# Kernel tuning notes

Hardware: AMD Instinct MI355X
Metric: run time of the kernel (lower is better)

Reference implementation:

```python
import jax, jax.numpy as jnp
import numpy as np

N = 2048       # num nodes
IN = 512       # in_features == hidden_features == out_features (residuals)
HID = 512
OUT = 512
H = 8          # num_heads
DX = 256       # x feature dim
LN_EPS = 1e-5
NORM_EPS = 1e-12


def _layernorm(x, g, b):
    mu = jnp.mean(x, axis=-1, keepdims=True)
    var = jnp.mean(jnp.square(x - mu), axis=-1, keepdims=True)
    return (x - mu) * jax.lax.rsqrt(var + LN_EPS) * g + b


def _l1_normalize(x):
    # torch F.normalize(p=1): x / max(||x||_1, eps)
    n = jnp.sum(jnp.abs(x), axis=-1, keepdims=True)
    return x / jnp.maximum(n, NORM_EPS)


def _linear_init(key, out_f, in_f):
    kw, kb = jax.random.split(key)
    bound = 1.0 / np.sqrt(in_f)
    W = jax.random.uniform(kw, (out_f, in_f), jnp.float32, -bound, bound)
    b = jax.random.uniform(kb, (out_f,), jnp.float32, -bound, bound)
    return W, b


def setup_inputs() -> dict:
    key = jax.random.key(0)
    ks = jax.random.split(key, 10)
    h = jax.random.normal(ks[0], (N, IN), jnp.float32)
    x = jax.random.uniform(ks[1], (N, DX), jnp.float32)
    Wk, bk = _linear_init(ks[2], HID, IN)
    Wq, bq = _linear_init(ks[3], HID, IN)
    Wv, bv = _linear_init(ks[4], HID, IN)
    Wm1, bm1 = _linear_init(ks[5], H, H + 1)   # mixing_x2h
    Wm2, bm2 = _linear_init(ks[6], 1, H)
    Wfc, bfc = _linear_init(ks[7], OUT, HID + 4)
    ln_g = jnp.ones((IN,), jnp.float32)
    ln_b = jnp.zeros((IN,), jnp.float32)
    lnf_g = jnp.ones((HID,), jnp.float32)
    lnf_b = jnp.zeros((HID,), jnp.float32)
    return dict(h=h, x=x, ln_g=ln_g, ln_b=ln_b, Wk=Wk, bk=bk, Wq=Wq, bq=bq,
                Wv=Wv, bv=bv, Wm1=Wm1, bm1=bm1, Wm2=Wm2, bm2=bm2,
                lnf_g=lnf_g, lnf_b=lnf_b, Wfc=Wfc, bfc=bfc)


def reference(h, x, ln_g, ln_b, Wk, bk, Wq, bq, Wv, bv, Wm1, bm1, Wm2, bm2,
              lnf_g, lnf_b, Wfc, bfc):
    h0, x0 = h, x
    hn = _layernorm(h, ln_g, ln_b)
    xn = _l1_normalize(x)

    k = (hn @ Wk.T + bk).reshape(N, HID // H, H)
    q = (hn @ Wq.T + bq).reshape(N, HID // H, H)
    a_h = jnp.einsum('xyb,zyb->xzb', k, q)          # [N, N, H]
    a_x = xn @ xn.T                                  # [N, N]

    # head mixing: Linear(H+1 -> H) over concat([a_x, a_h])
    a_cat = jnp.concatenate([a_x[..., None], a_h], axis=-1)  # [N, N, H+1]
    a_h = a_cat @ Wm1.T + bm1                                # [N, N, H]
    a_x = (a_h @ Wm2.T + bm2)[..., 0] + a_x                  # [N, N]

    a_h = jax.nn.softmax(a_h, axis=-1)               # softmax over heads
    a_x = _l1_normalize(a_x)

    # per-row stats of a_x -> [N, 4]
    i = jnp.concatenate([
        jnp.diagonal(a_x)[:, None],
        jnp.sum(a_x, axis=-1, keepdims=True),
        jnp.std(a_x, axis=-1, ddof=1, keepdims=True),
        jnp.max(a_x, axis=-1, keepdims=True),
    ], axis=-1)

    v = (hn @ Wv.T + bv).reshape(N, OUT // H, H)
    hm = jnp.einsum('xyb,yzb->xzb', a_h, v).reshape(N, HID)
    xm = a_x @ xn

    hm = hm + h0
    xm = xm + x0
    _h0 = hm

    hf = _layernorm(hm, lnf_g, lnf_b)
    hf = jnp.concatenate([hf, i], axis=-1)           # [N, HID+4]
    hf = jax.nn.elu(hf @ Wfc.T + bfc)
    hf = hf + _h0
    return (hf, xm)
```

## Files before the change

kernel.cpp:

```cpp
#include <hip/hip_runtime.h>
#include <math.h>

#define NN 2048
#define FD 512
#define DXF 256
#define JC 8
#define CHKJ (NN/JC)
#define ITI 32
#define JTW 64
#define NIT (CHKJ/JTW)
#define KC (NN/4)

typedef unsigned short u16;
typedef unsigned int u32;
typedef __attribute__((ext_vector_type(8))) short s16x8;
typedef __attribute__((ext_vector_type(4))) float f32x4;

__device__ __forceinline__ f32x4 MFMA16(s16x8 a, s16x8 b, f32x4 c) {
  return __builtin_amdgcn_mfma_f32_16x16x32_bf16(a, b, c, 0, 0, 0);
}
__device__ __forceinline__ float blo(u32 u) { return __uint_as_float(u << 16); }
__device__ __forceinline__ float bhi(u32 u) { return __uint_as_float(u & 0xffff0000u); }
__device__ __forceinline__ float b2f(u16 v) { return __uint_as_float((u32)v << 16); }
__device__ __forceinline__ u16 bf1(float f) {
  u32 u = __float_as_uint(f);
  u += 0x7fffu + ((u >> 16) & 1u);
  return (u16)(u >> 16);
}
__device__ __forceinline__ u32 pkbf(float a, float b) {
  u32 ua = __float_as_uint(a), ub = __float_as_uint(b);
  ua += 0x7fffu + ((ua >> 16) & 1u);
  ub += 0x7fffu + ((ub >> 16) & 1u);
  return (ua >> 16) | (ub & 0xffff0000u);
}

__global__ void preproc_k(
    const float* __restrict__ h, const float* __restrict__ ln_g,
    const float* __restrict__ ln_b, u16* __restrict__ hnB,
    const float* __restrict__ x, u16* __restrict__ xnB,
    const float* __restrict__ Wk, const float* __restrict__ Wq,
    const float* __restrict__ Wv, u16* __restrict__ wkB, u16* __restrict__ wqB,
    u16* __restrict__ wvB, const float* __restrict__ Wfc, u16* __restrict__ wfcB) {
  int bid = blockIdx.x, t = threadIdx.x;
  __shared__ float red[4][2];
  if (bid < NN) {
    int r = bid;
    float2 v = ((const float2*)(h + (size_t)r * FD))[t];
    float2 w = make_float2(v.x + v.y, v.x * v.x + v.y * v.y);
#pragma unroll
    for (int o = 32; o > 0; o >>= 1) { w.x += __shfl_xor(w.x, o); w.y += __shfl_xor(w.y, o); }
    if ((t & 63) == 0) { red[t >> 6][0] = w.x; red[t >> 6][1] = w.y; }
    __syncthreads();
    float S  = (red[0][0] + red[1][0]) + (red[2][0] + red[3][0]);
    float SQ = (red[0][1] + red[1][1]) + (red[2][1] + red[3][1]);
    float mean = S * (1.f / FD);
    float var  = SQ * (1.f / FD) - mean * mean;
    float rs = rsqrtf(var + 1e-5f);
    float2 gg = ((const float2*)ln_g)[t], bb = ((const float2*)ln_b)[t];
    float ox = (v.x - mean) * rs * gg.x + bb.x;
    float oy = (v.y - mean) * rs * gg.y + bb.y;
    *(u32*)(hnB + (size_t)r * FD + 2 * t) = pkbf(ox, oy);
  } else if (bid < 2 * NN) {
    int r = bid - NN;
    float v = x[(size_t)r * DXF + t];
    float s = fabsf(v);
#pragma unroll
    for (int o = 32; o > 0; o >>= 1) s += __shfl_xor(s, o);
    if ((t & 63) == 0) red[t >> 6][0] = s;
    __syncthreads();
    float S = (red[0][0] + red[1][0]) + (red[2][0] + red[3][0]);
    float inv = 1.f / fmaxf(S, 1e-12f);
    xnB[(size_t)r * DXF + t] = bf1(v * inv);
  } else if (bid < 2 * NN + 1536) {
    int idx = bid - 2 * NN;
    int z = idx >> 9;
    int i = ((idx & 511) << 8) + t;
    const float* W = (z == 0) ? Wk : (z == 1) ? Wq : Wv;
    u16* O = (z == 0) ? wkB : (z == 1) ? wqB : wvB;
    float2 v = ((const float2*)W)[i];
    ((u32*)O)[i] = pkbf(v.x, v.y);
  } else {
    int i = (bid - (2 * NN + 1536)) * 256 + t;
    if (i < 512 * 272) {
      int r = i / 272, c2 = (i - r * 272) * 2;
      float a = (c2 < 516) ? Wfc[r * 516 + c2] : 0.f;
      float b = (c2 + 1 < 516) ? Wfc[r * 516 + c2 + 1] : 0.f;
      ((u32*)wfcB)[i] = pkbf(a, b);
    }
  }
}

__global__ void xnt_k(const u16* __restrict__ xnB, u16* __restrict__ xnTg) {
  __shared__ u16 tile[16][264];
  int t = threadIdx.x;
  int r0 = blockIdx.x * 16;
#pragma unroll
  for (int s = 0; s < 2; ++s) {
    int c = s * 256 + t;
    int db = c & 31, row = c >> 5;
    *(uint4*)&tile[row][db * 8] = *(const uint4*)(xnB + (size_t)(r0 + row) * DXF + db * 8);
  }
  __syncthreads();
#pragma unroll
  for (int s = 0; s < 2; ++s) {
    int c = s * 256 + t;
    int jb = c & 1, d = c >> 1;
    u32 p[4];
#pragma unroll
    for (int e2 = 0; e2 < 4; ++e2) {
      u16 a = tile[jb * 8 + e2 * 2][d], b = tile[jb * 8 + e2 * 2 + 1][d];
      p[e2] = (u32)a | ((u32)b << 16);
    }
    *(uint4*)(xnTg + (size_t)d * NN + r0 + jb * 8) = make_uint4(p[0], p[1], p[2], p[3]);
  }
}

__global__ __launch_bounds__(256) void proj3_k(
    const u16* __restrict__ A,
    const u16* __restrict__ W0, const u16* __restrict__ W1, const u16* __restrict__ W2,
    const float* __restrict__ b0, const float* __restrict__ b1, const float* __restrict__ b2,
    u16* __restrict__ kP, u16* __restrict__ qP, u16* __restrict__ vPT) {
  int z = blockIdx.z;
  const u16* B = (z == 0) ? W0 : (z == 1) ? W1 : W2;
  const float* bias = (z == 0) ? b0 : (z == 1) ? b1 : b2;
  int t = threadIdx.x, w = t >> 6, lane = t & 63, g = lane >> 4, li = lane & 15;
  int m0 = blockIdx.x * 64 + (w & 1) * 32;
  int n0 = blockIdx.y * 64 + (w >> 1) * 32;
  f32x4 acc[2][2] = {};
  for (int k0 = 0; k0 < FD; k0 += 32) {
    s16x8 a0 = *(const s16x8*)(A + (size_t)(m0 + li) * FD + k0 + g * 8);
    s16x8 a1 = *(const s16x8*)(A + (size_t)(m0 + 16 + li) * FD + k0 + g * 8);
    s16x8 bA = *(const s16x8*)(B + (size_t)(n0 + li) * FD + k0 + g * 8);
    s16x8 bB = *(const s16x8*)(B + (size_t)(n0 + 16 + li) * FD + k0 + g * 8);
    acc[0][0] = MFMA16(a0, bA, acc[0][0]);
    acc[0][1] = MFMA16(a0, bB, acc[0][1]);
    acc[1][0] = MFMA16(a1, bA, acc[1][0]);
    acc[1][1] = MFMA16(a1, bB, acc[1][1]);
  }
#pragma unroll
  for (int ms = 0; ms < 2; ++ms)
#pragma unroll
    for (int ns = 0; ns < 2; ++ns) {
      int ncol = n0 + ns * 16 + li;
      float bv = bias[ncol];
      if (z < 2) {
        u16* out = z ? qP : kP;
#pragma unroll
        for (int r = 0; r < 4; ++r) {
          int i = m0 + ms * 16 + g * 4 + r;
          out[((size_t)(ncol & 7) * NN + i) * 64 + (ncol >> 3)] = bf1(acc[ms][ns][r] + bv);
        }
      } else {
        u16 e[4];
#pragma unroll
        for (int r = 0; r < 4; ++r) e[r] = bf1(acc[ms][ns][r] + bv);
        u32 p0 = (u32)e[0] | ((u32)e[1] << 16);
        u32 p1 = (u32)e[2] | ((u32)e[3] << 16);
        int ib = m0 + ms * 16 + g * 4;
        *(uint2*)(vPT + ((size_t)((ncol & 7) * 64 + (ncol >> 3))) * NN + ib) =
            make_uint2(p0, p1);
      }
    }
}

__global__ __launch_bounds__(256) void fc_gemm_k(
    const u16* __restrict__ A, const u16* __restrict__ B,
    const float* __restrict__ bias, const float* __restrict__ res,
    float* __restrict__ C) {
  int t = threadIdx.x, w = t >> 6, lane = t & 63, g = lane >> 4, li = lane & 15;
  int m0 = blockIdx.x * 32 + (w & 1) * 16;
  int n0 = blockIdx.y * 32 + (w >> 1) * 16;
  f32x4 acc = {};
  for (int k0 = 0; k0 < 544; k0 += 32) {
    s16x8 a0 = *(const s16x8*)(A + (size_t)(m0 + li) * 544 + k0 + g * 8);
    s16x8 b0 = *(const s16x8*)(B + (size_t)(n0 + li) * 544 + k0 + g * 8);
    acc = MFMA16(a0, b0, acc);
  }
  int ncol = n0 + li;
  float bv = bias[ncol];
#pragma unroll
  for (int r = 0; r < 4; ++r) {
    int i = m0 + g * 4 + r;
    float cv = acc[r] + bv;
    cv = (cv > 0.f) ? cv : (expf(cv) - 1.f);
    cv += res[(size_t)i * FD + ncol];
    C[(size_t)i * FD + ncol] = cv;
  }
}

__global__ __launch_bounds__(256) void xm_split_k(
    const u16* __restrict__ axg, const u16* __restrict__ xnTg,
    float* __restrict__ xmp, float* __restrict__ stq) {
  int t = threadIdx.x, w = t >> 6, lane = t & 63, g = lane >> 4, li = lane & 15;
  int m0 = blockIdx.x * 64 + (w & 1) * 32;
  int n0 = blockIdx.y * 64 + (w >> 1) * 32;
  int z = blockIdx.z;
  const int kb = z * KC;
  f32x4 acc[2][2] = {};
  float sab[2] = {0.f, 0.f}, ssu[2] = {0.f, 0.f}, ssq[2] = {0.f, 0.f};
  float smx[2] = {-1e30f, -1e30f};
  const bool do_stats = (blockIdx.y == 0) && ((w >> 1) == 0);
  for (int k0 = 0; k0 < KC; k0 += 32) {
    s16x8 a0 = *(const s16x8*)(axg + (size_t)(m0 + li) * NN + kb + k0 + g * 8);
    s16x8 a1 = *(const s16x8*)(axg + (size_t)(m0 + 16 + li) * NN + kb + k0 + g * 8);
    s16x8 bA = *(const s16x8*)(xnTg + (size_t)(n0 + li) * NN + kb + k0 + g * 8);
    s16x8 bB = *(const s16x8*)(xnTg + (size_t)(n0 + 16 + li) * NN + kb + k0 + g * 8);
    acc[0][0] = MFMA16(a0, bA, acc[0][0]);
    acc[0][1] = MFMA16(a0, bB, acc[0][1]);
    acc[1][0] = MFMA16(a1, bA, acc[1][0]);
    acc[1][1] = MFMA16(a1, bB, acc[1][1]);
    if (do_stats) {
#pragma unroll
      for (int ms = 0; ms < 2; ++ms) {
        u32 pu[4];
        *(s16x8*)pu = ms ? a1 : a0;
#pragma unroll
        for (int q2 = 0; q2 < 4; ++q2) {
          float x0 = blo(pu[q2]), x1 = bhi(pu[q2]);
          sab[ms] += fabsf(x0) + fabsf(x1);
          ssu[ms] += x0 + x1;
          ssq[ms] += x0 * x0 + x1 * x1;
          smx[ms] = fmaxf(smx[ms], fmaxf(x0, x1));
        }
      }
    }
  }
  if (do_stats) {
#pragma unroll
    for (int off = 16; off < 64; off <<= 1) {
#pragma unroll
      for (int ms = 0; ms < 2; ++ms) {
        sab[ms] += __shfl_xor(sab[ms], off);
        ssu[ms] += __shfl_xor(ssu[ms], off);
        ssq[ms] += __shfl_xor(ssq[ms], off);
        smx[ms] = fmaxf(smx[ms], __shfl_xor(smx[ms], off));
      }
    }
    if (g == 0) {
#pragma unroll
      for (int ms = 0; ms < 2; ++ms) {
        size_t base = ((size_t)z * NN + m0 + ms * 16 + li) * 4;
        stq[base + 0] = sab[ms]; stq[base + 1] = ssu[ms];
        stq[base + 2] = ssq[ms]; stq[base + 3] = smx[ms];
      }
    }
  }
#pragma unroll
  for (int ms = 0; ms < 2; ++ms)
#pragma unroll
    for (int ns = 0; ns < 2; ++ns) {
      int ncol = n0 + ns * 16 + li;
#pragma unroll
      for (int r = 0; r < 4; ++r) {
        int i = m0 + ms * 16 + g * 4 + r;
        xmp[(size_t)z * NN * DXF + (size_t)i * DXF + ncol] = acc[ms][ns][r];
      }
    }
}

__global__ __launch_bounds__(512, 4) void fused_mfma_k(
    const u16* __restrict__ kP, const u16* __restrict__ qP,
    const u16* __restrict__ vPT, const u16* __restrict__ xnB,
    const float* __restrict__ Wm1, const float* __restrict__ bm1,
    const float* __restrict__ Wm2, const float* __restrict__ bm2,
    u16* __restrict__ hmPart, u16* __restrict__ axg, float* __restrict__ stPd) {
  __shared__ __align__(16) unsigned char L[81920];
  const int O_KI = 0, O_XNI = 32768, O_P = 49152;
  const int t = threadIdx.x, w = t >> 6, lane = t & 63;
  const int g = lane >> 4, li = lane & 15;
  const int i0 = blockIdx.x * ITI, chunk = blockIdx.y;
  const int si = w & 1;
  const int jL = (w >> 1) * 16 + li;
  const int iRow = si * 16 + li;

  float W1[8][9], B1v[8], w2v[8];
#pragma unroll
  for (int o = 0; o < 8; ++o) {
    B1v[o] = bm1[o];
    w2v[o] = Wm2[o];
#pragma unroll
    for (int b3 = 0; b3 < 9; ++b3) W1[o][b3] = Wm1[o * 9 + b3];
  }
  const float b2v = bm2[0];

#pragma unroll
  for (int s = 0; s < 4; ++s) {
    int c = s * 512 + t;
    int yb = c & 7, il = (c >> 3) & 31, b = c >> 8;
    uint4 v = *(const uint4*)(kP + ((size_t)b * NN + i0 + il) * 64 + yb * 8);
    *(uint4*)(L + O_KI + b * 4096 + il * 128 + ((yb ^ (il & 7)) << 4)) = v;
  }
#pragma unroll
  for (int s = 0; s < 2; ++s) {
    int c = s * 512 + t;
    int db = c & 31, il = c >> 5;
    uint4 v = *(const uint4*)(xnB + (size_t)(i0 + il) * DXF + db * 8);
    *(uint4*)(L + O_XNI + il * 512 + ((db ^ (il & 7)) << 4)) = v;
  }
  __syncthreads();

  f32x4 hmA[2][4];
#pragma unroll
  for (int a = 0; a < 2; ++a)
#pragma unroll
    for (int c = 0; c < 4; ++c) hmA[a][c] = (f32x4)(0.f);

  for (int it = 0; it < NIT; ++it) {
    const int j0 = chunk * CHKJ + it * JTW;
    f32x4 accS[9];
#pragma unroll
    for (int a = 0; a < 9; ++a) accS[a] = (f32x4)(0.f);
#pragma unroll
    for (int b = 0; b < 8; ++b)
#pragma unroll
      for (int ks = 0; ks < 2; ++ks) {
        int blk = ks * 4 + g;
        s16x8 af = *(const s16x8*)(L + O_KI + b * 4096 + iRow * 128 +
                                   ((blk ^ (iRow & 7)) << 4));
        s16x8 bf = *(const s16x8*)(qP + ((size_t)b * NN + j0 + jL) * 64 + ks * 32 + g * 8);
        accS[b] = MFMA16(af, bf, accS[b]);
      }
#pragma unroll
    for (int ks = 0; ks < 8; ++ks) {
      int blk = ks * 4 + g;
      s16x8 af = *(const s16x8*)(L + O_XNI + iRow * 512 + ((blk ^ (iRow & 7)) << 4));
      s16x8 bf = *(const s16x8*)(xnB + (size_t)(j0 + jL) * DXF + ks * 32 + g * 8);
      accS[8] = MFMA16(af, bf, accS[8]);
    }
    __syncthreads();
#pragma unroll
    for (int r = 0; r < 4; ++r) {
      float sb[8];
#pragma unroll
      for (int b = 0; b < 8; ++b) sb[b] = accS[b][r];
      float ax = accS[8][r];
      float m[8];
#pragma unroll
      for (int o = 0; o < 8; ++o) {
        float a = B1v[o] + W1[o][0] * ax;
#pragma unroll
        for (int b = 0; b < 8; ++b) a += W1[o][1 + b] * sb[b];
        m[o] = a;
      }
      float axn = b2v + ax;
#pragma unroll
      for (int o = 0; o < 8; ++o) axn += w2v[o] * m[o];
      const int iL2 = si * 16 + g * 4 + r;
      const int iG = i0 + iL2, jG = j0 + jL;
      axg[(size_t)iG * NN + jG] = bf1(axn);
      if (iG == jG) stPd[iG] = axn;
      float mx = m[0];
#pragma unroll
      for (int o = 1; o < 8; ++o) mx = fmaxf(mx, m[o]);
      float es[8], esum = 0.f;
#pragma unroll
      for (int o = 0; o < 8; ++o) { es[o] = __expf(m[o] - mx); esum += es[o]; }
      float inv = 1.f / esum;
      const int base = iL2 * 128 + (((jL >> 3) ^ (iL2 & 7)) << 4) + (jL & 7) * 2;
#pragma unroll
      for (int b = 0; b < 8; ++b)
        *(u16*)(L + O_P + b * 4096 + base) = bf1(es[b] * inv);
    }
    __syncthreads();
#pragma unroll
    for (int hh = 0; hh < 2; ++hh) {
      const int hd = (w >> 1) * 2 + hh;
#pragma unroll
      for (int kb = 0; kb < 2; ++kb) {
        const int prow = si * 16 + li;
        s16x8 pa = *(const s16x8*)(L + O_P + hd * 4096 + prow * 128 +
                                   (((kb * 4 + g) ^ (prow & 7)) << 4));
#pragma unroll
        for (int zt = 0; zt < 4; ++zt) {
          s16x8 vf = *(const s16x8*)(vPT + ((size_t)hd * 64 + zt * 16 + li) * NN +
                                     j0 + kb * 32 + g * 8);
          hmA[hh][zt] = MFMA16(pa, vf, hmA[hh][zt]);
        }
      }
    }
  }
#pragma unroll
  for (int hh = 0; hh < 2; ++hh) {
    const int hd = (w >> 1) * 2 + hh;
#pragma unroll
    for (int zt = 0; zt < 4; ++zt)
#pragma unroll
      for (int r = 0; r < 4; ++r) {
        int i = i0 + si * 16 + g * 4 + r;
        int z = zt * 16 + li;
        hmPart[((size_t)(chunk * 8 + hd) * NN + i) * 64 + z] = bf1(hmA[hh][zt][r]);
      }
  }
}

__global__ void epilogue1_k(
    const float* __restrict__ h, const float* __restrict__ x,
    const u16* __restrict__ hmp, const float* __restrict__ xmp,
    const float* __restrict__ stq, const float* __restrict__ stPd,
    const float* __restrict__ lnf_g, const float* __restrict__ lnf_b,
    float* __restrict__ hmf, u16* __restrict__ hfeB, float* __restrict__ out_xm) {
  int r = blockIdx.x, t = threadIdx.x;
  int c0 = 2 * t, c1 = c0 + 1;
  float2 acc = ((const float2*)(h + (size_t)r * FD))[t];
#pragma unroll
  for (int ch = 0; ch < JC; ++ch) {
    acc.x += b2f(hmp[((size_t)(ch * 8 + (c0 & 7)) * NN + r) * 64 + (c0 >> 3)]);
    acc.y += b2f(hmp[((size_t)(ch * 8 + (c1 & 7)) * NN + r) * 64 + (c1 >> 3)]);
  }
  ((float2*)(hmf + (size_t)r * FD))[t] = acc;
  float2 w = make_float2(acc.x + acc.y, acc.x * acc.x + acc.y * acc.y);
#pragma unroll
  for (int o = 32; o > 0; o >>= 1) { w.x += __shfl_xor(w.x, o); w.y += __shfl_xor(w.y, o); }
  __shared__ float red[4][2];
  __shared__ float s_inv;
  if ((t & 63) == 0) { red[t >> 6][0] = w.x; red[t >> 6][1] = w.y; }
  __syncthreads();
  float S  = (red[0][0] + red[1][0]) + (red[2][0] + red[3][0]);
  float SQ = (red[0][1] + red[1][1]) + (red[2][1] + red[3][1]);
  float mean = S * (1.f / FD);
  float var  = SQ * (1.f / FD) - mean * mean;
  float rs = rsqrtf(var + 1e-5f);
  float2 g2 = ((const float2*)lnf_g)[t], b2 = ((const float2*)lnf_b)[t];
  float ox = (acc.x - mean) * rs * g2.x + b2.x;
  float oy = (acc.y - mean) * rs * g2.y + b2.y;
  *(u32*)(hfeB + (size_t)r * 544 + c0) = pkbf(ox, oy);
  if (t == 0) {
    float sab = 0.f, ssu = 0.f, ssq = 0.f, smx = -1e30f;
#pragma unroll
    for (int c = 0; c < 4; ++c) {
      size_t b = ((size_t)c * NN + r) * 4;
      sab += stq[b + 0]; ssu += stq[b + 1]; ssq += stq[b + 2];
      smx = fmaxf(smx, stq[b + 3]);
    }
    float diag = stPd[r];
    float L1 = fmaxf(sab, 1e-12f);
    float inv = 1.f / L1;
    float stdv = sqrtf(fmaxf((ssq - ssu * ssu * (1.f / 2048.f)) * (1.f / 2047.f), 0.f)) * inv;
    u16* he = hfeB + (size_t)r * 544;
    he[512] = bf1(diag * inv); he[513] = bf1(ssu * inv);
    he[514] = bf1(stdv);       he[515] = bf1(smx * inv);
    s_inv = inv;
  }
  if (t < 14) *(u32*)(hfeB + (size_t)r * 544 + 516 + 2 * t) = 0;
  __syncthreads();
  float inv = s_inv;
  float xv = xmp[(size_t)r * DXF + t] + xmp[(size_t)NN * DXF + (size_t)r * DXF + t] +
             xmp[2 * (size_t)NN * DXF + (size_t)r * DXF + t] +
             xmp[3 * (size_t)NN * DXF + (size_t)r * DXF + t];
  out_xm[(size_t)r * DXF + t] = xv * inv + x[(size_t)r * DXF + t];
}

extern "C" void kernel_launch(void* const* d_in, const int* in_sizes, int n_in,
                              void* d_out, int out_size, void* d_ws, size_t ws_size,
                              hipStream_t stream) {
  (void)in_sizes; (void)n_in; (void)out_size; (void)ws_size;
  const float* h    = (const float*)d_in[0];
  const float* x    = (const float*)d_in[1];
  const float* ln_g = (const float*)d_in[2];
  const float* ln_b = (const float*)d_in[3];
  const float* Wk   = (const float*)d_in[4];
  const float* bk   = (const float*)d_in[5];
  const float* Wq   = (const float*)d_in[6];
  const float* bq   = (const float*)d_in[7];
  const float* Wv   = (const float*)d_in[8];
  const float* bv   = (const float*)d_in[9];
  const float* Wm1  = (const float*)d_in[10];
  const float* bm1  = (const float*)d_in[11];
  const float* Wm2  = (const float*)d_in[12];
  const float* bm2  = (const float*)d_in[13];
  const float* lnf_g = (const float*)d_in[14];
  const float* lnf_b = (const float*)d_in[15];
  const float* Wfc  = (const float*)d_in[16];
  const float* bfc  = (const float*)d_in[17];

  char* wsb = (char*)d_ws;
  size_t off = 0;
  auto alloc = [&](size_t bytes) { char* p = wsb + off; off += (bytes + 255) & ~(size_t)255; return p; };
  u16*   hnB  = (u16*)alloc((size_t)NN * FD * 2);
  u16*   wkB  = (u16*)alloc((size_t)FD * FD * 2);
  u16*   wqB  = (u16*)alloc((size_t)FD * FD * 2);
  u16*   wvB  = (u16*)alloc((size_t)FD * FD * 2);
  u16*   wfcB = (u16*)alloc((size_t)512 * 544 * 2);
  u16*   kP   = (u16*)alloc((size_t)8 * NN * 64 * 2);
  u16*   qP   = (u16*)alloc((size_t)8 * NN * 64 * 2);
  u16*   vPT  = (u16*)alloc((size_t)8 * 64 * NN * 2);
  u16*   xnB  = (u16*)alloc((size_t)NN * DXF * 2);
  u16*   xnTg = (u16*)alloc((size_t)DXF * NN * 2);
  u16*   axg  = (u16*)alloc((size_t)NN * NN * 2);
  u16*   hmp  = (u16*)alloc((size_t)JC * 8 * NN * 64 * 2);
  float* xmp  = (float*)alloc((size_t)4 * NN * DXF * 4);
  float* stq  = (float*)alloc((size_t)4 * NN * 4 * 4);
  float* stPd = (float*)alloc((size_t)NN * 4);
  float* hmf  = (float*)alloc((size_t)NN * FD * 4);
  u16*   hfeB = (u16*)alloc((size_t)NN * 544 * 2);
  float* out_hf = (float*)d_out;
  float* out_xm = out_hf + (size_t)NN * FD;

  preproc_k<<<2 * NN + 1536 + 544, 256, 0, stream>>>(
      h, ln_g, ln_b, hnB, x, xnB, Wk, Wq, Wv, wkB, wqB, wvB, Wfc, wfcB);
  xnt_k<<<NN / 16, 256, 0, stream>>>(xnB, xnTg);

  proj3_k<<<dim3(32, 8, 3), 256, 0, stream>>>(hnB, wkB, wqB, wvB, bk, bq, bv, kP, qP, vPT);

  fused_mfma_k<<<dim3(NN / ITI, JC), 512, 0, stream>>>(kP, qP, vPT, xnB, Wm1, bm1, Wm2, bm2,
                                                       hmp, axg, stPd);

  xm_split_k<<<dim3(32, 4, 4), 256, 0, stream>>>(axg, xnTg, xmp, stq);

  epilogue1_k<<<NN, 256, 0, stream>>>(h, x, hmp, xmp, stq, stPd, lnf_g, lnf_b, hmf, hfeB, out_xm);

  fc_gemm_k<<<dim3(64, 16), 256, 0, stream>>>(hfeB, wfcB, bfc, hmf, out_hf);
}
```

Measured before the change: 168.7 us.

## Fuse xm GEMM and a_x row stats into the attention kernel

The pre-normalisation a_x tile is kept in shared memory and multiplied by xn inside the fused attention kernel, so the separate xm_split_k launch and the 2048x2048 bf16 axg round-trip through global memory go away. Row statistics (L1, sum, sum of squares, max) are taken from the fp32 values and reduced per block, then written per j-chunk. The k tile is now read straight from global memory instead of being staged in LDS, which cuts LDS use and may allow more blocks per CU. In exchange the attention kernel does more MFMA work and holds more registers, and the xm partials are stored as bf16 over eight chunks, which adds rounding error.

```diff
diff --git a/kernel.cpp b/kernel.cpp
--- a/kernel.cpp
+++ b/kernel.cpp
@@ -9,7 +9,6 @@
 #define ITI 32
 #define JTW 64
 #define NIT (CHKJ/JTW)
-#define KC (NN/4)
 
 typedef unsigned short u16;
 typedef unsigned int u32;
@@ -19,8 +18,6 @@
 __device__ __forceinline__ f32x4 MFMA16(s16x8 a, s16x8 b, f32x4 c) {
   return __builtin_amdgcn_mfma_f32_16x16x32_bf16(a, b, c, 0, 0, 0);
 }
-__device__ __forceinline__ float blo(u32 u) { return __uint_as_float(u << 16); }
-__device__ __forceinline__ float bhi(u32 u) { return __uint_as_float(u & 0xffff0000u); }
 __device__ __forceinline__ float b2f(u16 v) { return __uint_as_float((u32)v << 16); }
 __device__ __forceinline__ u16 bf1(float f) {
   u32 u = __float_as_uint(f);
@@ -188,89 +185,22 @@
   }
 }
 
-__global__ __launch_bounds__(256) void xm_split_k(
-    const u16* __restrict__ axg, const u16* __restrict__ xnTg,
-    float* __restrict__ xmp, float* __restrict__ stq) {
-  int t = threadIdx.x, w = t >> 6, lane = t & 63, g = lane >> 4, li = lane & 15;
-  int m0 = blockIdx.x * 64 + (w & 1) * 32;
-  int n0 = blockIdx.y * 64 + (w >> 1) * 32;
-  int z = blockIdx.z;
-  const int kb = z * KC;
-  f32x4 acc[2][2] = {};
-  float sab[2] = {0.f, 0.f}, ssu[2] = {0.f, 0.f}, ssq[2] = {0.f, 0.f};
-  float smx[2] = {-1e30f, -1e30f};
-  const bool do_stats = (blockIdx.y == 0) && ((w >> 1) == 0);
-  for (int k0 = 0; k0 < KC; k0 += 32) {
-    s16x8 a0 = *(const s16x8*)(axg + (size_t)(m0 + li) * NN + kb + k0 + g * 8);
-    s16x8 a1 = *(const s16x8*)(axg + (size_t)(m0 + 16 + li) * NN + kb + k0 + g * 8);
-    s16x8 bA = *(const s16x8*)(xnTg + (size_t)(n0 + li) * NN + kb + k0 + g * 8);
-    s16x8 bB = *(const s16x8*)(xnTg + (size_t)(n0 + 16 + li) * NN + kb + k0 + g * 8);
-    acc[0][0] = MFMA16(a0, bA, acc[0][0]);
-    acc[0][1] = MFMA16(a0, bB, acc[0][1]);
-    acc[1][0] = MFMA16(a1, bA, acc[1][0]);
-    acc[1][1] = MFMA16(a1, bB, acc[1][1]);
-    if (do_stats) {
-#pragma unroll
-      for (int ms = 0; ms < 2; ++ms) {
-        u32 pu[4];
-        *(s16x8*)pu = ms ? a1 : a0;
-#pragma unroll
-        for (int q2 = 0; q2 < 4; ++q2) {
-          float x0 = blo(pu[q2]), x1 = bhi(pu[q2]);
-          sab[ms] += fabsf(x0) + fabsf(x1);
-          ssu[ms] += x0 + x1;
-          ssq[ms] += x0 * x0 + x1 * x1;
-          smx[ms] = fmaxf(smx[ms], fmaxf(x0, x1));
-        }
-      }
-    }
-  }
-  if (do_stats) {
-#pragma unroll
-    for (int off = 16; off < 64; off <<= 1) {
-#pragma unroll
-      for (int ms = 0; ms < 2; ++ms) {
-        sab[ms] += __shfl_xor(sab[ms], off);
-        ssu[ms] += __shfl_xor(ssu[ms], off);
-        ssq[ms] += __shfl_xor(ssq[ms], off);
-        smx[ms] = fmaxf(smx[ms], __shfl_xor(smx[ms], off));
-      }
-    }
-    if (g == 0) {
-#pragma unroll
-      for (int ms = 0; ms < 2; ++ms) {
-        size_t base = ((size_t)z * NN + m0 + ms * 16 + li) * 4;
-        stq[base + 0] = sab[ms]; stq[base + 1] = ssu[ms];
-        stq[base + 2] = ssq[ms]; stq[base + 3] = smx[ms];
-      }
-    }
-  }
-#pragma unroll
-  for (int ms = 0; ms < 2; ++ms)
-#pragma unroll
-    for (int ns = 0; ns < 2; ++ns) {
-      int ncol = n0 + ns * 16 + li;
-#pragma unroll
-      for (int r = 0; r < 4; ++r) {
-        int i = m0 + ms * 16 + g * 4 + r;
-        xmp[(size_t)z * NN * DXF + (size_t)i * DXF + ncol] = acc[ms][ns][r];
-      }
-    }
-}
-
 __global__ __launch_bounds__(512, 4) void fused_mfma_k(
     const u16* __restrict__ kP, const u16* __restrict__ qP,
     const u16* __restrict__ vPT, const u16* __restrict__ xnB,
+    const u16* __restrict__ xnTg,
     const float* __restrict__ Wm1, const float* __restrict__ bm1,
     const float* __restrict__ Wm2, const float* __restrict__ bm2,
-    u16* __restrict__ hmPart, u16* __restrict__ axg, float* __restrict__ stPd) {
-  __shared__ __align__(16) unsigned char L[81920];
-  const int O_KI = 0, O_XNI = 32768, O_P = 49152;
+    u16* __restrict__ hmPart, u16* __restrict__ xmPart,
+    float* __restrict__ stq, float* __restrict__ stPd) {
+  __shared__ __align__(16) unsigned char L[53248];
+  const int O_XNI = 0, O_P = 16384, O_AXN = 49152;
   const int t = threadIdx.x, w = t >> 6, lane = t & 63;
   const int g = lane >> 4, li = lane & 15;
   const int i0 = blockIdx.x * ITI, chunk = blockIdx.y;
   const int si = w & 1;
-  const int jL = (w >> 1) * 16 + li;
+  const int jw = w >> 1;
+  const int jL = jw * 16 + li;
   const int iRow = si * 16 + li;
 
   float W1[8][9], B1v[8], w2v[8];
@@ -283,13 +213,6 @@
   }
   const float b2v = bm2[0];
 
-#pragma unroll
-  for (int s = 0; s < 4; ++s) {
-    int c = s * 512 + t;
-    int yb = c & 7, il = (c >> 3) & 31, b = c >> 8;
-    uint4 v = *(const uint4*)(kP + ((size_t)b * NN + i0 + il) * 64 + yb * 8);
-    *(uint4*)(L + O_KI + b * 4096 + il * 128 + ((yb ^ (il & 7)) << 4)) = v;
-  }
 #pragma unroll
   for (int s = 0; s < 2; ++s) {
     int c = s * 512 + t;
@@ -300,10 +223,15 @@
   __syncthreads();
 
   f32x4 hmA[2][4];
+  f32x4 xmA[4];
 #pragma unroll
   for (int a = 0; a < 2; ++a)
 #pragma unroll
     for (int c = 0; c < 4; ++c) hmA[a][c] = (f32x4)(0.f);
+#pragma unroll
+  for (int c = 0; c < 4; ++c) xmA[c] = (f32x4)(0.f);
+  float aab[4] = {0, 0, 0, 0}, asu[4] = {0, 0, 0, 0}, asq[4] = {0, 0, 0, 0};
+  float amx[4] = {-1e30f, -1e30f, -1e30f, -1e30f};
 
   for (int it = 0; it < NIT; ++it) {
     const int j0 = chunk * CHKJ + it * JTW;
@@ -314,9 +242,7 @@
     for (int b = 0; b < 8; ++b)
 #pragma unroll
       for (int ks = 0; ks < 2; ++ks) {
-        int blk = ks * 4 + g;
-        s16x8 af = *(const s16x8*)(L + O_KI + b * 4096 + iRow * 128 +
-                                   ((blk ^ (iRow & 7)) << 4));
+        s16x8 af = *(const s16x8*)(kP + ((size_t)b * NN + i0 + iRow) * 64 + ks * 32 + g * 8);
         s16x8 bf = *(const s16x8*)(qP + ((size_t)b * NN + j0 + jL) * 64 + ks * 32 + g * 8);
         accS[b] = MFMA16(af, bf, accS[b]);
       }
@@ -345,9 +271,10 @@
       float axn = b2v + ax;
 #pragma unroll
       for (int o = 0; o < 8; ++o) axn += w2v[o] * m[o];
+      aab[r] += fabsf(axn); asu[r] += axn; asq[r] += axn * axn;
+      amx[r] = fmaxf(amx[r], axn);
       const int iL2 = si * 16 + g * 4 + r;
       const int iG = i0 + iL2, jG = j0 + jL;
-      axg[(size_t)iG * NN + jG] = bf1(axn);
       if (iG == jG) stPd[iG] = axn;
       float mx = m[0];
 #pragma unroll
@@ -360,14 +287,15 @@
 #pragma unroll
       for (int b = 0; b < 8; ++b)
         *(u16*)(L + O_P + b * 4096 + base) = bf1(es[b] * inv);
+      *(u16*)(L + O_AXN + base) = bf1(axn);
     }
     __syncthreads();
+    const int prow = si * 16 + li;
 #pragma unroll
     for (int hh = 0; hh < 2; ++hh) {
-      const int hd = (w >> 1) * 2 + hh;
+      const int hd = jw * 2 + hh;
 #pragma unroll
       for (int kb = 0; kb < 2; ++kb) {
-        const int prow = si * 16 + li;
         s16x8 pa = *(const s16x8*)(L + O_P + hd * 4096 + prow * 128 +
                                    (((kb * 4 + g) ^ (prow & 7)) << 4));
 #pragma unroll
@@ -378,10 +306,21 @@
         }
       }
     }
+#pragma unroll
+    for (int kb = 0; kb < 2; ++kb) {
+      s16x8 xa = *(const s16x8*)(L + O_AXN + prow * 128 +
+                                 (((kb * 4 + g) ^ (prow & 7)) << 4));
+#pragma unroll
+      for (int ct = 0; ct < 4; ++ct) {
+        int cc = jw * 64 + ct * 16 + li;
+        s16x8 xb = *(const s16x8*)(xnTg + (size_t)cc * NN + j0 + kb * 32 + g * 8);
+        xmA[ct] = MFMA16(xa, xb, xmA[ct]);
+      }
+    }
   }
 #pragma unroll
   for (int hh = 0; hh < 2; ++hh) {
-    const int hd = (w >> 1) * 2 + hh;
+    const int hd = jw * 2 + hh;
 #pragma unroll
     for (int zt = 0; zt < 4; ++zt)
 #pragma unroll
@@ -391,11 +330,50 @@
         hmPart[((size_t)(chunk * 8 + hd) * NN + i) * 64 + z] = bf1(hmA[hh][zt][r]);
       }
   }
+#pragma unroll
+  for (int ct = 0; ct < 4; ++ct)
+#pragma unroll
+    for (int r = 0; r < 4; ++r) {
+      int i = i0 + si * 16 + g * 4 + r;
+      int cc = jw * 64 + ct * 16 + li;
+      xmPart[((size_t)chunk * NN + i) * DXF + cc] = bf1(xmA[ct][r]);
+    }
+#pragma unroll
+  for (int off = 1; off < 16; off <<= 1) {
+#pragma unroll
+    for (int r = 0; r < 4; ++r) {
+      aab[r] += __shfl_xor(aab[r], off);
+      asu[r] += __shfl_xor(asu[r], off);
+      asq[r] += __shfl_xor(asq[r], off);
+      amx[r] = fmaxf(amx[r], __shfl_xor(amx[r], off));
+    }
+  }
+  __syncthreads();
+  float* stL = (float*)(L + O_XNI);
+  if (li == 0) {
+#pragma unroll
+    for (int r = 0; r < 4; ++r) {
+      int iLoc = si * 16 + g * 4 + r;
+      float* p = stL + (iLoc * 4 + jw) * 4;
+      p[0] = aab[r]; p[1] = asu[r]; p[2] = asq[r]; p[3] = amx[r];
+    }
+  }
+  __syncthreads();
+  if (t < 32) {
+    float sab = 0.f, ssu = 0.f, ssq = 0.f, smx = -1e30f;
+#pragma unroll
+    for (int q = 0; q < 4; ++q) {
+      const float* p = stL + (t * 4 + q) * 4;
+      sab += p[0]; ssu += p[1]; ssq += p[2]; smx = fmaxf(smx, p[3]);
+    }
+    float* dst = stq + ((size_t)chunk * NN + i0 + t) * 4;
+    dst[0] = sab; dst[1] = ssu; dst[2] = ssq; dst[3] = smx;
+  }
 }
 
 __global__ void epilogue1_k(
     const float* __restrict__ h, const float* __restrict__ x,
-    const u16* __restrict__ hmp, const float* __restrict__ xmp,
+    const u16* __restrict__ hmp, const u16* __restrict__ xmb,
     const float* __restrict__ stq, const float* __restrict__ stPd,
     const float* __restrict__ lnf_g, const float* __restrict__ lnf_b,
     float* __restrict__ hmf, u16* __restrict__ hfeB, float* __restrict__ out_xm) {
@@ -427,10 +405,9 @@
   if (t == 0) {
     float sab = 0.f, ssu = 0.f, ssq = 0.f, smx = -1e30f;
 #pragma unroll
-    for (int c = 0; c < 4; ++c) {
-      size_t b = ((size_t)c * NN + r) * 4;
-      sab += stq[b + 0]; ssu += stq[b + 1]; ssq += stq[b + 2];
-      smx = fmaxf(smx, stq[b + 3]);
+    for (int c = 0; c < JC; ++c) {
+      const float* p = stq + ((size_t)c * NN + r) * 4;
+      sab += p[0]; ssu += p[1]; ssq += p[2]; smx = fmaxf(smx, p[3]);
     }
     float diag = stPd[r];
     float L1 = fmaxf(sab, 1e-12f);
@@ -444,9 +421,10 @@
   if (t < 14) *(u32*)(hfeB + (size_t)r * 544 + 516 + 2 * t) = 0;
   __syncthreads();
   float inv = s_inv;
-  float xv = xmp[(size_t)r * DXF + t] + xmp[(size_t)NN * DXF + (size_t)r * DXF + t] +
-             xmp[2 * (size_t)NN * DXF + (size_t)r * DXF + t] +
-             xmp[3 * (size_t)NN * DXF + (size_t)r * DXF + t];
+  float xv = 0.f;
+#pragma unroll
+  for (int ch = 0; ch < JC; ++ch)
+    xv += b2f(xmb[((size_t)ch * NN + r) * DXF + t]);
   out_xm[(size_t)r * DXF + t] = xv * inv + x[(size_t)r * DXF + t];
 }
 
@@ -486,10 +464,9 @@
   u16*   vPT  = (u16*)alloc((size_t)8 * 64 * NN * 2);
   u16*   xnB  = (u16*)alloc((size_t)NN * DXF * 2);
   u16*   xnTg = (u16*)alloc((size_t)DXF * NN * 2);
-  u16*   axg  = (u16*)alloc((size_t)NN * NN * 2);
   u16*   hmp  = (u16*)alloc((size_t)JC * 8 * NN * 64 * 2);
-  float* xmp  = (float*)alloc((size_t)4 * NN * DXF * 4);
-  float* stq  = (float*)alloc((size_t)4 * NN * 4 * 4);
+  u16*   xmb  = (u16*)alloc((size_t)JC * NN * DXF * 2);
+  float* stq  = (float*)alloc((size_t)JC * NN * 4 * 4);
   float* stPd = (float*)alloc((size_t)NN * 4);
   float* hmf  = (float*)alloc((size_t)NN * FD * 4);
   u16*   hfeB = (u16*)alloc((size_t)NN * 544 * 2);
@@ -502,12 +479,11 @@
 
   proj3_k<<<dim3(32, 8, 3), 256, 0, stream>>>(hnB, wkB, wqB, wvB, bk, bq, bv, kP, qP, vPT);
 
-  fused_mfma_k<<<dim3(NN / ITI, JC), 512, 0, stream>>>(kP, qP, vPT, xnB, Wm1, bm1, Wm2, bm2,
-                                                       hmp, axg, stPd);
-
-  xm_split_k<<<dim3(32, 4, 4), 256, 0, stream>>>(axg, xnTg, xmp, stq);
-
-  epilogue1_k<<<NN, 256, 0, stream>>>(h, x, hmp, xmp, stq, stPd, lnf_g, lnf_b, hmf, hfeB, out_xm);
+  fused_mfma_k<<<dim3(NN / ITI, JC), 512, 0, stream>>>(kP, qP, vPT, xnB, xnTg,
+                                                       Wm1, bm1, Wm2, bm2,
+                                                       hmp, xmb, stq, stPd);
+
+  epilogue1_k<<<NN, 256, 0, stream>>>(h, x, hmp, xmb, stq, stPd, lnf_g, lnf_b, hmf, hfeB, out_xm);
 
   fc_gemm_k<<<dim3(64, 16), 256, 0, stream>>>(hfeB, wfcB, bfc, hmf, out_hf);
 }
```

New measurement: 224.6 us. +33.1%, slower.

## Keep attention probabilities in registers and move row stats into fused kernel

Applied to the files above, without the earlier changes.

The fused attention kernel now computes the transposed score tile (j rows, i columns), so each lane holds four consecutive j values. The softmax probabilities can then feed a 16x16x16 MFMA directly from registers. This removes the LDS round trip and the syncs for the K/xn staging and the P matrix. Each wave keeps accumulators for all 8 heads and reduces them across j-waves through LDS at the end. The a_x row statistics are also computed in the fused kernel instead of in xm_split_k. The cost is much higher register pressure (occupancy hint lowered to 2), K and xn fragments loaded straight from global memory, and a cross-wave reduction epilogue.

```diff
diff --git a/kernel.cpp b/kernel.cpp
--- a/kernel.cpp
+++ b/kernel.cpp
@@ -14,13 +14,15 @@
 typedef unsigned short u16;
 typedef unsigned int u32;
 typedef __attribute__((ext_vector_type(8))) short s16x8;
+typedef __attribute__((ext_vector_type(4))) short s16x4;
 typedef __attribute__((ext_vector_type(4))) float f32x4;
 
 __device__ __forceinline__ f32x4 MFMA16(s16x8 a, s16x8 b, f32x4 c) {
   return __builtin_amdgcn_mfma_f32_16x16x32_bf16(a, b, c, 0, 0, 0);
 }
-__device__ __forceinline__ float blo(u32 u) { return __uint_as_float(u << 16); }
-__device__ __forceinline__ float bhi(u32 u) { return __uint_as_float(u & 0xffff0000u); }
+__device__ __forceinline__ f32x4 MFMA16K16(s16x4 a, s16x4 b, f32x4 c) {
+  return __builtin_amdgcn_mfma_f32_16x16x16bf16_1k(a, b, c, 0, 0, 0);
+}
 __device__ __forceinline__ float b2f(u16 v) { return __uint_as_float((u32)v << 16); }
 __device__ __forceinline__ u16 bf1(float f) {
   u32 u = __float_as_uint(f);
@@ -190,16 +192,13 @@
 
 __global__ __launch_bounds__(256) void xm_split_k(
     const u16* __restrict__ axg, const u16* __restrict__ xnTg,
-    float* __restrict__ xmp, float* __restrict__ stq) {
+    float* __restrict__ xmp) {
   int t = threadIdx.x, w = t >> 6, lane = t & 63, g = lane >> 4, li = lane & 15;
   int m0 = blockIdx.x * 64 + (w & 1) * 32;
   int n0 = blockIdx.y * 64 + (w >> 1) * 32;
   int z = blockIdx.z;
   const int kb = z * KC;
   f32x4 acc[2][2] = {};
-  float sab[2] = {0.f, 0.f}, ssu[2] = {0.f, 0.f}, ssq[2] = {0.f, 0.f};
-  float smx[2] = {-1e30f, -1e30f};
-  const bool do_stats = (blockIdx.y == 0) && ((w >> 1) == 0);
   for (int k0 = 0; k0 < KC; k0 += 32) {
     s16x8 a0 = *(const s16x8*)(axg + (size_t)(m0 + li) * NN + kb + k0 + g * 8);
     s16x8 a1 = *(const s16x8*)(axg + (size_t)(m0 + 16 + li) * NN + kb + k0 + g * 8);
@@ -209,41 +208,6 @@
     acc[0][1] = MFMA16(a0, bB, acc[0][1]);
     acc[1][0] = MFMA16(a1, bA, acc[1][0]);
     acc[1][1] = MFMA16(a1, bB, acc[1][1]);
-    if (do_stats) {
-#pragma unroll
-      for (int ms = 0; ms < 2; ++ms) {
-        u32 pu[4];
-        *(s16x8*)pu = ms ? a1 : a0;
-#pragma unroll
-        for (int q2 = 0; q2 < 4; ++q2) {
-          float x0 = blo(pu[q2]), x1 = bhi(pu[q2]);
-          sab[ms] += fabsf(x0) + fabsf(x1);
-          ssu[ms] += x0 + x1;
-          ssq[ms] += x0 * x0 + x1 * x1;
-          smx[ms] = fmaxf(smx[ms], fmaxf(x0, x1));
-        }
-      }
-    }
-  }
-  if (do_stats) {
-#pragma unroll
-    for (int off = 16; off < 64; off <<= 1) {
-#pragma unroll
-      for (int ms = 0; ms < 2; ++ms) {
-        sab[ms] += __shfl_xor(sab[ms], off);
-        ssu[ms] += __shfl_xor(ssu[ms], off);
-        ssq[ms] += __shfl_xor(ssq[ms], off);
-        smx[ms] = fmaxf(smx[ms], __shfl_xor(smx[ms], off));
-      }
-    }
-    if (g == 0) {
-#pragma unroll
-      for (int ms = 0; ms < 2; ++ms) {
-        size_t base = ((size_t)z * NN + m0 + ms * 16 + li) * 4;
-        stq[base + 0] = sab[ms]; stq[base + 1] = ssu[ms];
-        stq[base + 2] = ssq[ms]; stq[base + 3] = smx[ms];
-      }
-    }
   }
 #pragma unroll
   for (int ms = 0; ms < 2; ++ms)
@@ -258,20 +222,19 @@
     }
 }
 
-__global__ __launch_bounds__(512, 4) void fused_mfma_k(
+__global__ __launch_bounds__(512, 2) void fused_mfma_k(
     const u16* __restrict__ kP, const u16* __restrict__ qP,
     const u16* __restrict__ vPT, const u16* __restrict__ xnB,
     const float* __restrict__ Wm1, const float* __restrict__ bm1,
     const float* __restrict__ Wm2, const float* __restrict__ bm2,
-    u16* __restrict__ hmPart, u16* __restrict__ axg, float* __restrict__ stPd) {
-  __shared__ __align__(16) unsigned char L[81920];
-  const int O_KI = 0, O_XNI = 32768, O_P = 49152;
+    u16* __restrict__ hmPart, u16* __restrict__ axg,
+    float* __restrict__ stq, float* __restrict__ stPd) {
+  __shared__ __align__(16) float LF[8 * 16 * 64];
   const int t = threadIdx.x, w = t >> 6, lane = t & 63;
   const int g = lane >> 4, li = lane & 15;
+  const int si = w >> 2, jw = w & 3;
   const int i0 = blockIdx.x * ITI, chunk = blockIdx.y;
-  const int si = w & 1;
-  const int jL = (w >> 1) * 16 + li;
-  const int iRow = si * 16 + li;
+  const int iR = i0 + si * 16 + li;
 
   float W1[8][9], B1v[8], w2v[8];
 #pragma unroll
@@ -283,30 +246,15 @@
   }
   const float b2v = bm2[0];
 
-#pragma unroll
-  for (int s = 0; s < 4; ++s) {
-    int c = s * 512 + t;
-    int yb = c & 7, il = (c >> 3) & 31, b = c >> 8;
-    uint4 v = *(const uint4*)(kP + ((size_t)b * NN + i0 + il) * 64 + yb * 8);
-    *(uint4*)(L + O_KI + b * 4096 + il * 128 + ((yb ^ (il & 7)) << 4)) = v;
-  }
-#pragma unroll
-  for (int s = 0; s < 2; ++s) {
-    int c = s * 512 + t;
-    int db = c & 31, il = c >> 5;
-    uint4 v = *(const uint4*)(xnB + (size_t)(i0 + il) * DXF + db * 8);
-    *(uint4*)(L + O_XNI + il * 512 + ((db ^ (il & 7)) << 4)) = v;
-  }
-  __syncthreads();
-
-  f32x4 hmA[2][4];
-#pragma unroll
-  for (int a = 0; a < 2; ++a)
+  f32x4 hmA[8][4];
+#pragma unroll
+  for (int a = 0; a < 8; ++a)
 #pragma unroll
     for (int c = 0; c < 4; ++c) hmA[a][c] = (f32x4)(0.f);
+  float aab = 0.f, asu = 0.f, asq = 0.f, amx = -1e30f;
 
   for (int it = 0; it < NIT; ++it) {
-    const int j0 = chunk * CHKJ + it * JTW;
+    const int jb = chunk * CHKJ + it * JTW + jw * 16;
     f32x4 accS[9];
 #pragma unroll
     for (int a = 0; a < 9; ++a) accS[a] = (f32x4)(0.f);
@@ -314,20 +262,17 @@
     for (int b = 0; b < 8; ++b)
 #pragma unroll
       for (int ks = 0; ks < 2; ++ks) {
-        int blk = ks * 4 + g;
-        s16x8 af = *(const s16x8*)(L + O_KI + b * 4096 + iRow * 128 +
-                                   ((blk ^ (iRow & 7)) << 4));
-        s16x8 bf = *(const s16x8*)(qP + ((size_t)b * NN + j0 + jL) * 64 + ks * 32 + g * 8);
+        s16x8 af = *(const s16x8*)(qP + ((size_t)b * NN + jb + li) * 64 + ks * 32 + g * 8);
+        s16x8 bf = *(const s16x8*)(kP + ((size_t)b * NN + iR) * 64 + ks * 32 + g * 8);
         accS[b] = MFMA16(af, bf, accS[b]);
       }
 #pragma unroll
     for (int ks = 0; ks < 8; ++ks) {
-      int blk = ks * 4 + g;
-      s16x8 af = *(const s16x8*)(L + O_XNI + iRow * 512 + ((blk ^ (iRow & 7)) << 4));
-      s16x8 bf = *(const s16x8*)(xnB + (size_t)(j0 + jL) * DXF + ks * 32 + g * 8);
+      s16x8 af = *(const s16x8*)(xnB + (size_t)(jb + li) * DXF + ks * 32 + g * 8);
+      s16x8 bf = *(const s16x8*)(xnB + (size_t)iR * DXF + ks * 32 + g * 8);
       accS[8] = MFMA16(af, bf, accS[8]);
     }
-    __syncthreads();
+    u16 pb[9][4];
 #pragma unroll
     for (int r = 0; r < 4; ++r) {
       float sb[8];
@@ -345,10 +290,9 @@
       float axn = b2v + ax;
 #pragma unroll
       for (int o = 0; o < 8; ++o) axn += w2v[o] * m[o];
-      const int iL2 = si * 16 + g * 4 + r;
-      const int iG = i0 + iL2, jG = j0 + jL;
-      axg[(size_t)iG * NN + jG] = bf1(axn);
-      if (iG == jG) stPd[iG] = axn;
+      aab += fabsf(axn); asu += axn; asq += axn * axn; amx = fmaxf(amx, axn);
+      int jG = jb + g * 4 + r;
+      if (iR == jG) stPd[iR] = axn;
       float mx = m[0];
 #pragma unroll
       for (int o = 1; o < 8; ++o) mx = fmaxf(mx, m[o]);
@@ -356,40 +300,64 @@
 #pragma unroll
       for (int o = 0; o < 8; ++o) { es[o] = __expf(m[o] - mx); esum += es[o]; }
       float inv = 1.f / esum;
-      const int base = iL2 * 128 + (((jL >> 3) ^ (iL2 & 7)) << 4) + (jL & 7) * 2;
-#pragma unroll
-      for (int b = 0; b < 8; ++b)
-        *(u16*)(L + O_P + b * 4096 + base) = bf1(es[b] * inv);
-    }
+#pragma unroll
+      for (int o = 0; o < 8; ++o) pb[o][r] = bf1(es[o] * inv);
+      pb[8][r] = bf1(axn);
+    }
+    {
+      s16x4 av = {(short)pb[8][0], (short)pb[8][1], (short)pb[8][2], (short)pb[8][3]};
+      *(s16x4*)(axg + (size_t)iR * NN + jb + g * 4) = av;
+    }
+#pragma unroll
+    for (int hd = 0; hd < 8; ++hd) {
+      s16x4 pa = {(short)pb[hd][0], (short)pb[hd][1], (short)pb[hd][2], (short)pb[hd][3]};
+#pragma unroll
+      for (int zt = 0; zt < 4; ++zt) {
+        s16x4 vb = *(const s16x4*)(vPT + (size_t)(hd * 64 + zt * 16 + li) * NN + jb + g * 4);
+        hmA[hd][zt] = MFMA16K16(pa, vb, hmA[hd][zt]);
+      }
+    }
+  }
+
+  for (int hd = 0; hd < 8; ++hd) {
     __syncthreads();
 #pragma unroll
-    for (int hh = 0; hh < 2; ++hh) {
-      const int hd = (w >> 1) * 2 + hh;
-#pragma unroll
-      for (int kb = 0; kb < 2; ++kb) {
-        const int prow = si * 16 + li;
-        s16x8 pa = *(const s16x8*)(L + O_P + hd * 4096 + prow * 128 +
-                                   (((kb * 4 + g) ^ (prow & 7)) << 4));
-#pragma unroll
-        for (int zt = 0; zt < 4; ++zt) {
-          s16x8 vf = *(const s16x8*)(vPT + ((size_t)hd * 64 + zt * 16 + li) * NN +
-                                     j0 + kb * 32 + g * 8);
-          hmA[hh][zt] = MFMA16(pa, vf, hmA[hh][zt]);
-        }
-      }
-    }
-  }
-#pragma unroll
-  for (int hh = 0; hh < 2; ++hh) {
-    const int hd = (w >> 1) * 2 + hh;
-#pragma unroll
     for (int zt = 0; zt < 4; ++zt)
 #pragma unroll
-      for (int r = 0; r < 4; ++r) {
-        int i = i0 + si * 16 + g * 4 + r;
-        int z = zt * 16 + li;
-        hmPart[((size_t)(chunk * 8 + hd) * NN + i) * 64 + z] = bf1(hmA[hh][zt][r]);
-      }
+      for (int r = 0; r < 4; ++r)
+        LF[(w * 16 + g * 4 + r) * 64 + zt * 16 + li] = hmA[hd][zt][r];
+    __syncthreads();
+#pragma unroll
+    for (int u = 0; u < 4; ++u) {
+      int flat = u * 512 + t;
+      int si2 = flat >> 10, rest = flat & 1023, ii = rest >> 6, zz = rest & 63;
+      float s = LF[((si2 * 4 + 0) * 16 + ii) * 64 + zz] +
+                LF[((si2 * 4 + 1) * 16 + ii) * 64 + zz] +
+                LF[((si2 * 4 + 2) * 16 + ii) * 64 + zz] +
+                LF[((si2 * 4 + 3) * 16 + ii) * 64 + zz];
+      hmPart[((size_t)(chunk * 8 + hd) * NN + i0 + si2 * 16 + ii) * 64 + zz] = bf1(s);
+    }
+  }
+  aab += __shfl_xor(aab, 16); aab += __shfl_xor(aab, 32);
+  asu += __shfl_xor(asu, 16); asu += __shfl_xor(asu, 32);
+  asq += __shfl_xor(asq, 16); asq += __shfl_xor(asq, 32);
+  amx = fmaxf(amx, __shfl_xor(amx, 16)); amx = fmaxf(amx, __shfl_xor(amx, 32));
+  __syncthreads();
+  if (lane < 16) {
+    float* p = LF + (w * 16 + li) * 4;
+    p[0] = aab; p[1] = asu; p[2] = asq; p[3] = amx;
+  }
+  __syncthreads();
+  if (t < 32) {
+    int si2 = t >> 4, il = t & 15;
+    float sab = 0.f, ssu = 0.f, ssq = 0.f, smx = -1e30f;
+#pragma unroll
+    for (int q = 0; q < 4; ++q) {
+      const float* p = LF + ((si2 * 4 + q) * 16 + il) * 4;
+      sab += p[0]; ssu += p[1]; ssq += p[2]; smx = fmaxf(smx, p[3]);
+    }
+    float* dst = stq + ((size_t)chunk * NN + i0 + t) * 4;
+    dst[0] = sab; dst[1] = ssu; dst[2] = ssq; dst[3] = smx;
   }
 }
 
@@ -427,10 +395,9 @@
   if (t == 0) {
     float sab = 0.f, ssu = 0.f, ssq = 0.f, smx = -1e30f;
 #pragma unroll
-    for (int c = 0; c < 4; ++c) {
-      size_t b = ((size_t)c * NN + r) * 4;
-      sab += stq[b + 0]; ssu += stq[b + 1]; ssq += stq[b + 2];
-      smx = fmaxf(smx, stq[b + 3]);
+    for (int c = 0; c < JC; ++c) {
+      const float* p = stq + ((size_t)c * NN + r) * 4;
+      sab += p[0]; ssu += p[1]; ssq += p[2]; smx = fmaxf(smx, p[3]);
     }
     float diag = stPd[r];
     float L1 = fmaxf(sab, 1e-12f);
@@ -489,7 +456,7 @@
   u16*   axg  = (u16*)alloc((size_t)NN * NN * 2);
   u16*   hmp  = (u16*)alloc((size_t)JC * 8 * NN * 64 * 2);
   float* xmp  = (float*)alloc((size_t)4 * NN * DXF * 4);
-  float* stq  = (float*)alloc((size_t)4 * NN * 4 * 4);
+  float* stq  = (float*)alloc((size_t)JC * NN * 4 * 4);
   float* stPd = (float*)alloc((size_t)NN * 4);
   float* hmf  = (float*)alloc((size_t)NN * FD * 4);
   u16*   hfeB = (u16*)alloc((size_t)NN * 544 * 2);
@@ -502,10 +469,11 @@
 
   proj3_k<<<dim3(32, 8, 3), 256, 0, stream>>>(hnB, wkB, wqB, wvB, bk, bq, bv, kP, qP, vPT);
 
-  fused_mfma_k<<<dim3(NN / ITI, JC), 512, 0, stream>>>(kP, qP, vPT, xnB, Wm1, bm1, Wm2, bm2,
-                                                       hmp, axg, stPd);
-
-  xm_split_k<<<dim3(32, 4, 4), 256, 0, stream>>>(axg, xnTg, xmp, stq);
+  fused_mfma_k<<<dim3(NN / ITI, JC), 512, 0, stream>>>(kP, qP, vPT, xnB,
+                                                       Wm1, bm1, Wm2, bm2,
+                                                       hmp, axg, stq, stPd);
+
+  xm_split_k<<<dim3(32, 4, 4), 256, 0, stream>>>(axg, xnTg, xmp);
 
   epilogue1_k<<<NN, 256, 0, stream>>>(h, x, hmp, xmp, stq, stPd, lnf_g, lnf_b, hmf, hfeB, out_xm);
 
```

Result: slower. 281.8 us (+67.1%).
